# Performance work log

Measured on AMD Instinct MI355X. Metric: run time of the kernel, lower is better.

Reference implementation:

```python
import jax, jax.numpy as jnp
import numpy as np

KH, KW = 3, 3
PAD = 1
C_IN, C_OUT = 64, 128


def unfold(x, kh, kw, pad):
    # x: (B, C, H, W) -> (B, C, kh*kw, H*W), torch.nn.functional.unfold ordering
    B, C, H, W = x.shape
    xp = jnp.pad(x, ((0, 0), (0, 0), (pad, pad), (pad, pad)))
    patches = jnp.stack(
        [xp[:, :, i:i + H, j:j + W] for i in range(kh) for j in range(kw)],
        axis=2,
    )  # (B, C, K, H, W)
    return patches.reshape(B, C, kh * kw, H * W)


def setup_inputs() -> dict:
    key = jax.random.key(0)
    k1, k2, k3 = jax.random.split(key, 3)
    B, H, W = 8, 128, 128
    inp = jax.random.normal(k1, (B, C_IN, H, W), dtype=jnp.float32)
    g_buffer = jax.random.uniform(k2, (B, 2, H, W), dtype=jnp.float32)
    # weights param as in torch: (1, C*kh*kw, 1, out_channels), kaiming-uniform-ish
    wdepth = C_IN * KH * KW
    bound = float(np.sqrt(6.0 / wdepth))
    weights = jax.random.uniform(k3, (1, wdepth, 1, C_OUT), dtype=jnp.float32,
                                 minval=-bound, maxval=bound)
    bias = jnp.zeros((C_OUT,), dtype=jnp.float32)
    return {"input": inp, "g_buffer": g_buffer, "weights": weights, "bias": bias}


def reference(input, g_buffer, weights, bias):
    B, C, H, W = input.shape
    K = KH * KW
    L = H * W
    depth = 2.0 * (g_buffer[:, -1:, :, :] - 0.5)  # (B, 1, H, W)

    input_unf = unfold(input, KH, KW, PAD)          # (B, C, K, L)
    depth_unf = unfold(depth, KH, KW, PAD)          # (B, 1, K, L)

    # bilateral depth weighting
    dfeat = depth_unf - depth.reshape(B, 1, 1, L)   # (B, 1, K, L)
    dfeat = jnp.sum(dfeat * dfeat, axis=1)          # (B, K, L)
    wf = jnp.exp(-dfeat)
    wf = 9.0 * wf / jnp.sum(wf, axis=1, keepdims=True)  # (B, K, L)

    filt = input_unf * wf[:, None, :, :]            # (B, C, K, L)
    filt = filt.reshape(B, C * K, L)

    W2 = weights.reshape(C_OUT, C * K)              # raw reshape, matches torch .view
    out_unf = jnp.einsum('bkl,ok->bol', filt, W2)   # (B, C_OUT, L)
    out = out_unf.reshape(B, C_OUT, H, W) + bias[None, :, None, None]
    return out
```

## Files before the change

kernel.cpp:

```cpp
#include <hip/hip_runtime.h>
#include <hip/hip_bf16.h>
#include <stdint.h>

typedef _Float16 f16x8 __attribute__((ext_vector_type(8)));
typedef float    f32x4 __attribute__((ext_vector_type(4)));

#define CIN   64
#define COUT  128
#define HH    128
#define WW    128
#define BB    8

#define TROW  130
#define ROWBYTES (130 * 128)
#define TSIZE ((size_t)BB * TROW * ROWBYTES)


__global__ void prep_weights(const float* __restrict__ wflat, _Float16* __restrict__ bp) {
    int idx = blockIdx.x * 256 + threadIdx.x;
    if (idx >= 8 * 18 * 64 * 8) return;
    int j = idx & 7;
    int l = (idx >> 3) & 63;
    int s = (idx >> 9) % 18;
    int n = idx / (18 * 512);
    int o = n * 16 + (l & 15);
    int c = ((s & 1) << 5) + ((l >> 4) << 3) + j;
    int k = s >> 1;
    bp[idx] = (_Float16)wflat[o * 576 + c * 9 + k];
}

__global__ void zero_halo(_Float16* __restrict__ T) {
    int idx = blockIdx.x * 256 + threadIdx.x;
    if (idx >= 16 * 1040) return;
    int row = idx / 1040, c = idx - row * 1040;
    int b = row >> 1, yp = (row & 1) * 129;
    f16x8 z = {};
    *(f16x8*)((char*)T + (size_t)(b * TROW + yp) * ROWBYTES + c * 16) = z;
}

__global__ __launch_bounds__(256) void transpose_pass(const float* __restrict__ inp,
                                                      _Float16* __restrict__ T) {
    __shared__ float sT[64][129];
    const int b   = blockIdx.x >> 7;
    const int y   = blockIdx.x & 127;
    const int tid = threadIdx.x;

    const float* ib = inp + ((long)b * CIN * HH + y) * WW;
    const int xq = tid & 31, c8 = tid >> 5;
    #pragma unroll
    for (int i = 0; i < 8; ++i) {
        int c = c8 * 8 + i;
        float4 v = *(const float4*)(ib + (long)c * (HH * WW) + (xq << 2));
        *(float4*)&sT[c][xq << 2] = v;
    }
    __syncthreads();

    const int x  = tid & 127;
    const int ch = tid >> 7;
    char* rowp = (char*)T + (size_t)(b * TROW + y + 1) * ROWBYTES + (size_t)(x + 1) * 128;
    const int sw = (x + 1) & 7;
    for (int c0 = ch * 8; c0 < 64; c0 += 16) {
        f16x8 v;
        #pragma unroll
        for (int j = 0; j < 8; ++j) v[j] = (_Float16)sT[c0 + j][x];
        *(f16x8*)(rowp + (((c0 >> 3) ^ sw) << 4)) = v;
    }
    if (tid < 16) {
        char* basep = (char*)T + (size_t)(b * TROW + y + 1) * ROWBYTES
                    + ((tid >> 3) ? 129 * 128 : 0) + (tid & 7) * 16;
        f16x8 z = {};
        *(f16x8*)basep = z;
    }
}

__global__ __launch_bounds__(512, 2) void depthcnn_main(
    const _Float16* __restrict__ T, const float* __restrict__ gbuf,
    const float* __restrict__ bias, const _Float16* __restrict__ aprep,
    float* __restrict__ out)
{
    __shared__ __align__(1024) char sIn[6 * ROWBYTES];
    __shared__ _Float16 sWf[4][WW][16];

    const int b      = blockIdx.x >> 5;
    const int ystart = (blockIdx.x & 31) << 2;
    const int tid    = threadIdx.x;
    const int wave   = tid >> 6;
    const int lane   = tid & 63;
    const int oi     = wave >> 1;
    const int pi     = wave & 1;
    const int l15    = lane & 15;
    const int g4     = lane >> 4;
    const int pxbase = pi << 6;

    const char* Tb = (const char*)T + (size_t)b * TROW * ROWBYTES;

    {
        const char* src = Tb + (size_t)ystart * ROWBYTES;
        for (int t = tid; t < 6 * 1040; t += 512)
            __builtin_amdgcn_global_load_lds(
                (const __attribute__((address_space(1))) uint32_t*)(src + (size_t)t * 16),
                (__attribute__((address_space(3))) uint32_t*)(sIn + t * 16), 16, 0, 0);
    }

    {
        const int r = tid >> 7, x = tid & 127, y = ystart + r;
        const float* g = gbuf + ((size_t)b * 2 + 1) * (HH * WW);
        float dc = 2.f * (g[y * WW + x] - 0.5f);
        float e[9];
        float ssum = 0.f;
        #pragma unroll
        for (int k = 0; k < 9; ++k) {
            int yy = y + (k / 3) - 1;
            int xx = x + (k % 3) - 1;
            float dn = 0.f;
            if ((unsigned)yy < 128u && (unsigned)xx < 128u)
                dn = 2.f * (g[yy * WW + xx] - 0.5f);
            float df = dn - dc;
            float ek = __expf(-df * df);
            e[k] = ek;
            ssum += ek;
        }
        float sc = 9.f / ssum;
        #pragma unroll
        for (int k = 0; k < 9; ++k) sWf[r][x][k] = (_Float16)(e[k] * sc);
    }

    f16x8 afr[2][18];
    {
        const f16x8* ap = (const f16x8*)aprep;
        #pragma unroll
        for (int t2 = 0; t2 < 2; ++t2)
            #pragma unroll
            for (int s = 0; s < 18; ++s)
                afr[t2][s] = ap[(size_t)(((oi * 2 + t2) * 18) + s) * 64 + lane];
    }
    float bv[2][4];
    #pragma unroll
    for (int t2 = 0; t2 < 2; ++t2)
        #pragma unroll
        for (int r4 = 0; r4 < 4; ++r4)
            bv[t2][r4] = bias[(oi << 5) + (t2 << 4) + (g4 << 2) + r4];

    __syncthreads();

    float* ob0 = out + (size_t)b * COUT * HH * WW;

    #pragma unroll 1
    for (int r = 0; r < 4; ++r) {
        const int y = ystart + r;

        f16x8    w07[4];
        _Float16 w8s[4];
        #pragma unroll
        for (int pt = 0; pt < 4; ++pt) {
            const int px = pxbase + (pt << 4) + l15;
            w07[pt] = *(const f16x8*)&sWf[r][px][0];
            w8s[pt] = sWf[r][px][8];
        }

        f32x4 acc[2][4];
        #pragma unroll
        for (int t2 = 0; t2 < 2; ++t2)
            #pragma unroll
            for (int pt = 0; pt < 4; ++pt)
                acc[t2][pt] = (f32x4){0.f, 0.f, 0.f, 0.f};

        #pragma unroll
        for (int s = 0; s < 18; ++s) {
            const int k  = s >> 1;
            const int ch = s & 1;
            const int dy = k / 3;
            const int dx = k - 3 * dy;
            const int rowb = (r + dy) * ROWBYTES;
            f16x8 bfrg[4];
            #pragma unroll
            for (int pt = 0; pt < 4; ++pt) {
                const int xp  = pxbase + (pt << 4) + l15 + dx;
                const int off = rowb + (xp << 7) + ((((ch << 2) | g4) ^ (xp & 7)) << 4);
                f16x8 iv = *(const f16x8*)(sIn + off);
                _Float16 wh = (k < 8) ? w07[pt][k] : w8s[pt];
                f16x8 w8 = {wh, wh, wh, wh, wh, wh, wh, wh};
                bfrg[pt] = iv * w8;
            }
            #pragma unroll
            for (int t2 = 0; t2 < 2; ++t2)
                #pragma unroll
                for (int pt = 0; pt < 4; ++pt)
                    acc[t2][pt] = __builtin_amdgcn_mfma_f32_16x16x32_f16(
                        afr[t2][s], bfrg[pt], acc[t2][pt], 0, 0, 0);
        }

        #pragma unroll
        for (int t2 = 0; t2 < 2; ++t2) {
            #pragma unroll
            for (int pt = 0; pt < 4; ++pt) {
                #pragma unroll
                for (int r4 = 0; r4 < 4; ++r4) {
                    const int o  = (oi << 5) + (t2 << 4) + (g4 << 2) + r4;
                    const int px = pxbase + (pt << 4) + l15;
                    ob0[(size_t)o * (HH * WW) + (size_t)y * WW + px] = acc[t2][pt][r4] + bv[t2][r4];
                }
            }
        }
    }
}

extern "C" void kernel_launch(void* const* d_in, const int* in_sizes, int n_in,
                              void* d_out, int out_size, void* d_ws, size_t ws_size,
                              hipStream_t stream) {
    const float* inp  = (const float*)d_in[0];
    const float* gbuf = (const float*)d_in[1];
    const float* wts  = (const float*)d_in[2];
    const float* bias = (const float*)d_in[3];

    _Float16* T  = (_Float16*)d_ws;
    _Float16* bp = (_Float16*)((char*)d_ws + TSIZE);

    hipLaunchKernelGGL(zero_halo, dim3(65), dim3(256), 0, stream, T);
    hipLaunchKernelGGL(transpose_pass, dim3(BB * HH), dim3(256), 0, stream, inp, T);
    hipLaunchKernelGGL(prep_weights, dim3(288), dim3(256), 0, stream, wts, bp);
    hipLaunchKernelGGL(depthcnn_main, dim3(256), dim3(512), 0, stream,
                       T, gbuf, bias, bp, (float*)d_out);
}
```

Before: 51.00 us.

## Split main kernel into half-width tiles, stream weights per step, fuse prep kernels

The main conv kernel now covers a 64-pixel half-row tile per block, which doubles the grid from 256 to 512 blocks and roughly halves LDS use per block. Launch bounds rise to allow 4 blocks per CU. Weight fragments are no longer held in registers for the whole kernel; each MFMA step loads them from global memory (expected to hit L2), which lowers register pressure in exchange for extra loads inside the inner loop. Weight prep and halo zeroing are merged into one kernel, saving a launch.

```diff
diff --git a/kernel.cpp b/kernel.cpp
--- a/kernel.cpp
+++ b/kernel.cpp
@@ -15,27 +15,31 @@
 #define ROWBYTES (130 * 128)
 #define TSIZE ((size_t)BB * TROW * ROWBYTES)
 
-
-__global__ void prep_weights(const float* __restrict__ wflat, _Float16* __restrict__ bp) {
-    int idx = blockIdx.x * 256 + threadIdx.x;
-    if (idx >= 8 * 18 * 64 * 8) return;
-    int j = idx & 7;
-    int l = (idx >> 3) & 63;
-    int s = (idx >> 9) % 18;
-    int n = idx / (18 * 512);
-    int o = n * 16 + (l & 15);
-    int c = ((s & 1) << 5) + ((l >> 4) << 3) + j;
-    int k = s >> 1;
-    bp[idx] = (_Float16)wflat[o * 576 + c * 9 + k];
-}
-
-__global__ void zero_halo(_Float16* __restrict__ T) {
-    int idx = blockIdx.x * 256 + threadIdx.x;
-    if (idx >= 16 * 1040) return;
-    int row = idx / 1040, c = idx - row * 1040;
-    int b = row >> 1, yp = (row & 1) * 129;
-    f16x8 z = {};
-    *(f16x8*)((char*)T + (size_t)(b * TROW + yp) * ROWBYTES + c * 16) = z;
+#define XH    66
+#define HROWB (XH * 128)
+
+
+__global__ void prep_plus(const float* __restrict__ wflat, _Float16* __restrict__ bp,
+                          _Float16* __restrict__ T) {
+    int gid = blockIdx.x * 256 + threadIdx.x;
+    if (gid < 8 * 18 * 64 * 8) {
+        int j = gid & 7;
+        int l = (gid >> 3) & 63;
+        int s = (gid >> 9) % 18;
+        int n = gid / (18 * 512);
+        int o = n * 16 + (l & 15);
+        int c = ((s & 1) << 5) + ((l >> 4) << 3) + j;
+        int k = s >> 1;
+        bp[gid] = (_Float16)wflat[o * 576 + c * 9 + k];
+        return;
+    }
+    int h = gid - 8 * 18 * 64 * 8;
+    if (h < 16 * 1040) {
+        int row = h / 1040, c = h - row * 1040;
+        int b = row >> 1, yp = (row & 1) * 129;
+        f16x8 z = {};
+        *(f16x8*)((char*)T + (size_t)(b * TROW + yp) * ROWBYTES + c * 16) = z;
+    }
 }
 
 __global__ __launch_bounds__(256) void transpose_pass(const float* __restrict__ inp,
@@ -73,16 +77,18 @@
     }
 }
 
-__global__ __launch_bounds__(512, 2) void depthcnn_main(
+__global__ __launch_bounds__(512, 4) void depthcnn_main(
     const _Float16* __restrict__ T, const float* __restrict__ gbuf,
     const float* __restrict__ bias, const _Float16* __restrict__ aprep,
     float* __restrict__ out)
 {
-    __shared__ __align__(1024) char sIn[6 * ROWBYTES];
-    __shared__ _Float16 sWf[4][WW][16];
-
-    const int b      = blockIdx.x >> 5;
-    const int ystart = (blockIdx.x & 31) << 2;
+    __shared__ __align__(1024) char sIn[6 * HROWB];
+    __shared__ _Float16 sWf[4][64][16];
+
+    const int blk    = blockIdx.x;
+    const int b      = blk >> 6;
+    const int ystart = ((blk >> 1) & 31) << 2;
+    const int x0     = (blk & 1) << 6;
     const int tid    = threadIdx.x;
     const int wave   = tid >> 6;
     const int lane   = tid & 63;
@@ -90,20 +96,19 @@
     const int pi     = wave & 1;
     const int l15    = lane & 15;
     const int g4     = lane >> 4;
-    const int pxbase = pi << 6;
-
-    const char* Tb = (const char*)T + (size_t)b * TROW * ROWBYTES;
 
     {
-        const char* src = Tb + (size_t)ystart * ROWBYTES;
-        for (int t = tid; t < 6 * 1040; t += 512)
-            __builtin_amdgcn_global_load_lds(
-                (const __attribute__((address_space(1))) uint32_t*)(src + (size_t)t * 16),
-                (__attribute__((address_space(3))) uint32_t*)(sIn + t * 16), 16, 0, 0);
-    }
-
-    {
-        const int r = tid >> 7, x = tid & 127, y = ystart + r;
+        const char* src = (const char*)T + ((size_t)b * TROW + ystart) * ROWBYTES + (size_t)x0 * 128;
+        #pragma unroll
+        for (int r6 = 0; r6 < 6; ++r6)
+            for (int c = tid; c < 528; c += 512)
+                __builtin_amdgcn_global_load_lds(
+                    (const __attribute__((address_space(1))) uint32_t*)(src + (size_t)r6 * ROWBYTES + c * 16),
+                    (__attribute__((address_space(3))) uint32_t*)(sIn + r6 * HROWB + c * 16), 16, 0, 0);
+    }
+
+    if (tid < 256) {
+        const int r = tid >> 6, pxl = tid & 63, x = x0 + pxl, y = ystart + r;
         const float* g = gbuf + ((size_t)b * 2 + 1) * (HH * WW);
         float dc = 2.f * (g[y * WW + x] - 0.5f);
         float e[9];
@@ -122,18 +127,9 @@
         }
         float sc = 9.f / ssum;
         #pragma unroll
-        for (int k = 0; k < 9; ++k) sWf[r][x][k] = (_Float16)(e[k] * sc);
-    }
-
-    f16x8 afr[2][18];
-    {
-        const f16x8* ap = (const f16x8*)aprep;
-        #pragma unroll
-        for (int t2 = 0; t2 < 2; ++t2)
-            #pragma unroll
-            for (int s = 0; s < 18; ++s)
-                afr[t2][s] = ap[(size_t)(((oi * 2 + t2) * 18) + s) * 64 + lane];
-    }
+        for (int k = 0; k < 9; ++k) sWf[r][pxl][k] = (_Float16)(e[k] * sc);
+    }
+
     float bv[2][4];
     #pragma unroll
     for (int t2 = 0; t2 < 2; ++t2)
@@ -143,26 +139,27 @@
 
     __syncthreads();
 
+    const f16x8* __restrict__ ap = (const f16x8*)aprep;
     float* ob0 = out + (size_t)b * COUT * HH * WW;
 
     #pragma unroll 1
     for (int r = 0; r < 4; ++r) {
         const int y = ystart + r;
 
-        f16x8    w07[4];
-        _Float16 w8s[4];
-        #pragma unroll
-        for (int pt = 0; pt < 4; ++pt) {
-            const int px = pxbase + (pt << 4) + l15;
-            w07[pt] = *(const f16x8*)&sWf[r][px][0];
-            w8s[pt] = sWf[r][px][8];
-        }
-
-        f32x4 acc[2][4];
+        f16x8    w07[2];
+        _Float16 w8s[2];
+        #pragma unroll
+        for (int pt = 0; pt < 2; ++pt) {
+            const int pxl = (pi << 5) + (pt << 4) + l15;
+            w07[pt] = *(const f16x8*)&sWf[r][pxl][0];
+            w8s[pt] = sWf[r][pxl][8];
+        }
+
+        f32x4 acc[2][2];
         #pragma unroll
         for (int t2 = 0; t2 < 2; ++t2)
             #pragma unroll
-            for (int pt = 0; pt < 4; ++pt)
+            for (int pt = 0; pt < 2; ++pt)
                 acc[t2][pt] = (f32x4){0.f, 0.f, 0.f, 0.f};
 
         #pragma unroll
@@ -171,12 +168,18 @@
             const int ch = s & 1;
             const int dy = k / 3;
             const int dx = k - 3 * dy;
-            const int rowb = (r + dy) * ROWBYTES;
-            f16x8 bfrg[4];
-            #pragma unroll
-            for (int pt = 0; pt < 4; ++pt) {
-                const int xp  = pxbase + (pt << 4) + l15 + dx;
-                const int off = rowb + (xp << 7) + ((((ch << 2) | g4) ^ (xp & 7)) << 4);
+            const int rowb = (r + dy) * HROWB;
+
+            f16x8 wfr[2];
+            #pragma unroll
+            for (int t2 = 0; t2 < 2; ++t2)
+                wfr[t2] = ap[(size_t)(((oi * 2 + t2) * 18) + s) * 64 + lane];
+
+            f16x8 bfrg[2];
+            #pragma unroll
+            for (int pt = 0; pt < 2; ++pt) {
+                const int xl  = (pi << 5) + (pt << 4) + l15 + dx;
+                const int off = rowb + (xl << 7) + ((((ch << 2) | g4) ^ (xl & 7)) << 4);
                 f16x8 iv = *(const f16x8*)(sIn + off);
                 _Float16 wh = (k < 8) ? w07[pt][k] : w8s[pt];
                 f16x8 w8 = {wh, wh, wh, wh, wh, wh, wh, wh};
@@ -185,19 +188,19 @@
             #pragma unroll
             for (int t2 = 0; t2 < 2; ++t2)
                 #pragma unroll
-                for (int pt = 0; pt < 4; ++pt)
+                for (int pt = 0; pt < 2; ++pt)
                     acc[t2][pt] = __builtin_amdgcn_mfma_f32_16x16x32_f16(
-                        afr[t2][s], bfrg[pt], acc[t2][pt], 0, 0, 0);
+                        wfr[t2], bfrg[pt], acc[t2][pt], 0, 0, 0);
         }
 
         #pragma unroll
         for (int t2 = 0; t2 < 2; ++t2) {
             #pragma unroll
-            for (int pt = 0; pt < 4; ++pt) {
+            for (int pt = 0; pt < 2; ++pt) {
                 #pragma unroll
                 for (int r4 = 0; r4 < 4; ++r4) {
                     const int o  = (oi << 5) + (t2 << 4) + (g4 << 2) + r4;
-                    const int px = pxbase + (pt << 4) + l15;
+                    const int px = x0 + (pi << 5) + (pt << 4) + l15;
                     ob0[(size_t)o * (HH * WW) + (size_t)y * WW + px] = acc[t2][pt][r4] + bv[t2][r4];
                 }
             }
@@ -216,9 +219,8 @@
     _Float16* T  = (_Float16*)d_ws;
     _Float16* bp = (_Float16*)((char*)d_ws + TSIZE);
 
-    hipLaunchKernelGGL(zero_halo, dim3(65), dim3(256), 0, stream, T);
+    hipLaunchKernelGGL(prep_plus, dim3(353), dim3(256), 0, stream, wts, bp, T);
     hipLaunchKernelGGL(transpose_pass, dim3(BB * HH), dim3(256), 0, stream, inp, T);
-    hipLaunchKernelGGL(prep_weights, dim3(288), dim3(256), 0, stream, wts, bp);
-    hipLaunchKernelGGL(depthcnn_main, dim3(256), dim3(512), 0, stream,
+    hipLaunchKernelGGL(depthcnn_main, dim3(512), dim3(512), 0, stream,
                        T, gbuf, bias, bp, (float*)d_out);
 }
```

Result: slower. 99.13 us (+94.4%).
